# Kernel optimization log

Measured on AMD Instinct MI355X. Metric: run time of the kernel, lower is better.

Reference implementation:

```python
import jax, jax.numpy as jnp
import numpy as np
from jax import lax

T, D = 8192, 128          # sequence length, feature dim
N_INIT = 100              # burn-in length
RENORM = 0.1
A, B, C = 0.5, 0.9, 0.1   # weighted_dot scaling args: uv = A*gram + B*k_prev + C
EPS = 1e-6                # keep arcsin arg strictly inside (-1, 1)


def kernel_fn(uv, uu, vv):
    # erf-network arcsin kernel
    denom = jnp.sqrt((1.0 + 2.0 * uu) * (1.0 + 2.0 * vv))
    arg = jnp.clip(2.0 * uv / denom, -1.0 + EPS, 1.0 - EPS)
    return (2.0 / jnp.pi) * jnp.arcsin(arg)


def dot_fn(g, k):
    return A * g + B * k + C


def setup_inputs() -> dict:
    key = jax.random.key(0)
    data = jax.random.normal(key, (T, D), dtype=jnp.float32) / np.float32(np.sqrt(D))
    return {"data": data}


def reference(data):
    X = data[:-1]                      # [N, D], N = T - 1
    N = X.shape[0]
    gram = jnp.dot(X, X.T)             # [N, N]
    diag = jnp.diag(gram)              # [N]

    # --- diagonal recursion: scalar carry over time ---
    def diag_step(k_prev, g):
        uv = dot_fn(g, k_prev)
        k = kernel_fn(uv, uv, uv)
        return k, k

    k_diag_final, k_diag = lax.scan(diag_step, jnp.float32(0.0), diag)
    k_diag_shift = jnp.pad(k_diag[:-1], (1, 0))   # shift by one step
    uu = dot_fn(diag, k_diag_shift)               # [N]

    # --- full kernel recursion: carry is a length-N row, shifted each step ---
    def row_step(k_prev, inputs):
        g_row, vv = inputs
        k_prev = jnp.pad(k_prev[:-1], (1, 0))
        uv = dot_fn(g_row, k_prev)
        k = kernel_fn(uv, uu, vv)
        return k, k

    k_final, k_train = lax.scan(row_step, jnp.zeros((N,), jnp.float32), (gram, uu))

    k_train = k_train[N_INIT - 1:, N_INIT - 1:] + RENORM * gram[N_INIT - 1:, N_INIT - 1:]
    return (k_train, uu, k_final, k_diag_final)
```

## Files before the change

kernel.cpp:

```cpp
#include <hip/hip_runtime.h>
#include <hip/hip_fp16.h>

#define N_ROWS 8191
#define NO 8092
#define GSTRIDE 8192
#define SEG 512
#define WARM 96

#define OUT_UU  65480464ul
#define OUT_KF  65488655ul
#define OUT_KDF 65496846ul

#define WS_XB   134217728ul
#define WS_DIAG 136314880ul
#define WS_Q    136347648ul

typedef short bf16x8 __attribute__((ext_vector_type(8)));
typedef float f32x4  __attribute__((ext_vector_type(4)));

__device__ __forceinline__ float asin_core(float a) {
    float ax  = fabsf(a);
    bool  big = ax > 0.5f;
    float z   = big ? 0.5f * (1.0f - ax) : ax * ax;
    float x   = big ? sqrtf(z) : ax;
    float p = fmaf(z, 4.2163199048e-2f, 2.4181311049e-2f);
    p = fmaf(p, z, 4.5470025998e-2f);
    p = fmaf(p, z, 7.4953002686e-2f);
    p = fmaf(p, z, 1.6666752422e-1f);
    p = fmaf(p * z, x, x);
    float r = big ? fmaf(-2.0f, p, 1.57079632679489662f) : p;
    return copysignf(r, a);
}

__device__ __forceinline__ float kstep(float g, float kp, float m) {
    float uv  = fmaf(0.5f, g, fmaf(0.9f, kp, 0.1f));
    float arg = uv * m;
    arg = fminf(fmaxf(arg, -0.999999f), 0.999999f);
    return 0.63661977236758134f * asin_core(arg);
}

__device__ __forceinline__ unsigned short f2bf(float f) {
    unsigned int u = __float_as_uint(f);
    u = (u + 0x7FFFu + ((u >> 16) & 1u)) >> 16;
    return (unsigned short)u;
}

__global__ void k_convert(const float* __restrict__ X, unsigned short* __restrict__ Xb) {
    int idx = blockIdx.x * 256 + threadIdx.x;
    float v = (idx < N_ROWS * 128) ? X[idx] : 0.0f;
    Xb[idx] = f2bf(v);
}

__global__ void k_diag(const float* __restrict__ X, float* __restrict__ diag) {
    int gwave = (blockIdx.x * 256 + threadIdx.x) >> 6;
    int lane  = threadIdx.x & 63;
    if (gwave >= N_ROWS) return;
    const float2* row = (const float2*)(X + (size_t)gwave * 128);
    float2 v = row[lane];
    float s = v.x * v.x + v.y * v.y;
    #pragma unroll
    for (int off = 32; off > 0; off >>= 1) s += __shfl_xor(s, off, 64);
    if (lane == 0) diag[gwave] = s;
}

__global__ void k_scan_diag(const float* __restrict__ diag, float* __restrict__ q,
                            float* __restrict__ d_out) {
    int tid = threadIdx.x;
    int t0  = tid * 32;
    int tw  = max(0, t0 - 32);
    int te  = min(t0 + 32, N_ROWS);
    float kp = 0.0f;
    for (int t = tw; t < te; ++t) {
        float dg = diag[t];
        float uv = fmaf(0.5f, dg, fmaf(0.9f, kp, 0.1f));
        float s  = fabsf(fmaf(2.0f, uv, 1.0f));
        float arg = (uv + uv) / s;
        arg = fminf(fmaxf(arg, -0.999999f), 0.999999f);
        float k = 0.63661977236758134f * asin_core(arg);
        if (t >= t0) {
            d_out[OUT_UU + t] = uv;
            q[t] = 1.0f / sqrtf(s);
            if (t == N_ROWS - 1) d_out[OUT_KDF] = k;
        }
        kp = k;
    }
}

#define GP 136
__global__ __launch_bounds__(256) void k_gemm(const unsigned short* __restrict__ Xb,
                                              __half* __restrict__ gram) {
    int bi = blockIdx.y, bj = blockIdx.x;
    if (bj < bi) return;
    __shared__ short As[128 * GP];
    __shared__ short Bs[128 * GP];
    int tid = threadIdx.x;
    const uint4* ga = (const uint4*)(Xb + (size_t)bi * 128 * 128);
    const uint4* gb = (const uint4*)(Xb + (size_t)bj * 128 * 128);
    #pragma unroll
    for (int p = 0; p < 8; ++p) {
        int chunk = tid + p * 256;
        int row = chunk >> 4, c8 = chunk & 15;
        uint4 va = ga[row * 16 + c8];
        *(uint4*)&As[row * GP + c8 * 8] = va;
        uint4 vb = gb[row * 16 + c8];
        *(uint4*)&Bs[row * GP + c8 * 8] = vb;
    }
    __syncthreads();

    int lane = tid & 63, wave = tid >> 6;
    int wm = wave & 1, wn = wave >> 1;
    int lr = lane & 15, lk = lane >> 4;
    f32x4 acc[4][4];
    #pragma unroll
    for (int mi = 0; mi < 4; ++mi)
        #pragma unroll
        for (int ni = 0; ni < 4; ++ni) acc[mi][ni] = (f32x4){0.f, 0.f, 0.f, 0.f};

    #pragma unroll
    for (int kc = 0; kc < 4; ++kc) {
        bf16x8 a[4], b[4];
        #pragma unroll
        for (int mi = 0; mi < 4; ++mi)
            a[mi] = *(bf16x8*)&As[(wm * 64 + mi * 16 + lr) * GP + kc * 32 + lk * 8];
        #pragma unroll
        for (int ni = 0; ni < 4; ++ni)
            b[ni] = *(bf16x8*)&Bs[(wn * 64 + ni * 16 + lr) * GP + kc * 32 + lk * 8];
        #pragma unroll
        for (int mi = 0; mi < 4; ++mi)
            #pragma unroll
            for (int ni = 0; ni < 4; ++ni)
                acc[mi][ni] = __builtin_amdgcn_mfma_f32_16x16x32_bf16(a[mi], b[ni], acc[mi][ni], 0, 0, 0);
    }

    int row0 = (lane >> 4) * 4, col = lane & 15;
    #pragma unroll
    for (int mi = 0; mi < 4; ++mi) {
        #pragma unroll
        for (int ni = 0; ni < 4; ++ni) {
            size_t gi = (size_t)bi * 128 + wm * 64 + mi * 16 + row0;
            size_t gj = (size_t)bj * 128 + wn * 64 + ni * 16 + col;
            f32x4 v = acc[mi][ni];
            #pragma unroll
            for (int r = 0; r < 4; ++r)
                gram[(gi + r) * GSTRIDE + gj] = __float2half(v[r]);
        }
    }
}

__global__ __launch_bounds__(256) void k_scan_main(const __half* __restrict__ gram,
                                                   const float* __restrict__ q,
                                                   float* __restrict__ d_out) {
    int c = blockIdx.x * 256 + threadIdx.x;
    if (c > NO - 1) return;
    int tlim = N_ROWS - c;
    int t0 = 99 + blockIdx.y * SEG;
    if (t0 >= tlim) return;
    int tend = min(t0 + SEG, tlim);
    int tw = t0 - WARM;

    float kp = 0.0f;
    size_t gidx = (size_t)tw * GSTRIDE + tw + c;
    #pragma unroll 4
    for (int t = tw; t < t0; ++t, gidx += (GSTRIDE + 1)) {
        float g = __half2float(gram[gidx]);
        float m = 2.0f * q[t] * q[t + c];
        kp = kstep(g, kp, m);
    }
    size_t oidx = (size_t)(t0 - 99) * NO + (t0 + c - 99);
    #pragma unroll 4
    for (int t = t0; t < tend; ++t, gidx += (GSTRIDE + 1), oidx += (NO + 1)) {
        float g = __half2float(gram[gidx]);
        float m = 2.0f * q[t] * q[t + c];
        kp = kstep(g, kp, m);
        d_out[oidx] = fmaf(0.1f, g, kp);
    }
    if (tend == tlim) d_out[OUT_KF + (tlim - 1)] = kp;
}

__global__ void k_short_diag(const __half* __restrict__ gram, const float* __restrict__ q,
                             float* __restrict__ d_out) {
    int l = threadIdx.x;
    if (l > 98) return;
    int c = NO + l;
    int tl = N_ROWS - c;
    float kp = 0.0f;
    size_t gidx = (size_t)c;
    for (int t = 0; t < tl; ++t, gidx += (GSTRIDE + 1)) {
        float g = __half2float(gram[gidx]);
        float m = 2.0f * q[t] * q[t + c];
        kp = kstep(g, kp, m);
    }
    d_out[OUT_KF + (tl - 1)] = kp;
}

__global__ __launch_bounds__(256) void k_mirror(float* __restrict__ out) {
    int tc = blockIdx.x, tr = blockIdx.y;
    if (tr < tc) return;
    __shared__ float tile[32][33];
    int tx = threadIdx.x, ty = threadIdx.y;
    int sr0 = tc * 32, sc0 = tr * 32;
    #pragma unroll
    for (int k2 = 0; k2 < 32; k2 += 8) {
        int r = sr0 + ty + k2, cc = sc0 + tx;
        if (r < NO && cc < NO)
            tile[ty + k2][tx] = out[(size_t)r * NO + cc];
    }
    __syncthreads();
    int dr0 = tr * 32, dc0 = tc * 32;
    #pragma unroll
    for (int k2 = 0; k2 < 32; k2 += 8) {
        int r = dr0 + ty + k2, cc = dc0 + tx;
        if (r < NO && cc < NO && r > cc)
            out[(size_t)r * NO + cc] = tile[tx][ty + k2];
    }
}

extern "C" void kernel_launch(void* const* d_in, const int* in_sizes, int n_in,
                              void* d_out, int out_size, void* d_ws, size_t ws_size,
                              hipStream_t stream) {
    const float* X = (const float*)d_in[0];
    float* out = (float*)d_out;
    char* ws = (char*)d_ws;
    __half* gram = (__half*)ws;
    unsigned short* Xb = (unsigned short*)(ws + WS_XB);
    float* diag = (float*)(ws + WS_DIAG);
    float* q = (float*)(ws + WS_Q);

    k_convert<<<dim3(4096), dim3(256), 0, stream>>>(X, Xb);
    k_diag<<<dim3(2048), dim3(256), 0, stream>>>(X, diag);
    k_scan_diag<<<dim3(1), dim3(256), 0, stream>>>(diag, q, out);
    k_gemm<<<dim3(64, 64), dim3(256), 0, stream>>>(Xb, gram);
    k_scan_main<<<dim3(32, 16), dim3(256), 0, stream>>>(gram, q, out);
    k_short_diag<<<dim3(1), dim3(128), 0, stream>>>(gram, q, out);
    k_mirror<<<dim3(253, 253), dim3(32, 8), 0, stream>>>(out);
}
```

Measured before the change: 531.0 us.

## Fuse mirror write into scan via shared-memory transpose; merge convert and diag kernels

The scan kernel now stages its outputs in shared memory per 32-step chunk and writes the transposed lower-triangle entries directly. This removes the separate full-matrix mirror pass that re-read and rewrote the output. The bf16 conversion and diagonal norm kernels are merged into one launch, the factor of 2 is folded into q, and the warm-up length is halved. The costs are extra syncthreads and shared-memory traffic inside the scan, and a shorter warm-up that may lose accuracy.

```diff
diff --git a/kernel.cpp b/kernel.cpp
--- a/kernel.cpp
+++ b/kernel.cpp
@@ -5,7 +5,10 @@
 #define NO 8092
 #define GSTRIDE 8192
 #define SEG 512
-#define WARM 96
+#define WARM 48
+#define CHUNK 32
+#define LPAD 33
+#define LROWS (CHUNK + 255)
 
 #define OUT_UU  65480464ul
 #define OUT_KF  65488655ul
@@ -45,22 +48,23 @@
     return (unsigned short)u;
 }
 
-__global__ void k_convert(const float* __restrict__ X, unsigned short* __restrict__ Xb) {
-    int idx = blockIdx.x * 256 + threadIdx.x;
-    float v = (idx < N_ROWS * 128) ? X[idx] : 0.0f;
-    Xb[idx] = f2bf(v);
-}
-
-__global__ void k_diag(const float* __restrict__ X, float* __restrict__ diag) {
-    int gwave = (blockIdx.x * 256 + threadIdx.x) >> 6;
-    int lane  = threadIdx.x & 63;
-    if (gwave >= N_ROWS) return;
-    const float2* row = (const float2*)(X + (size_t)gwave * 128);
+__global__ void k_prep(const float* __restrict__ X, unsigned short* __restrict__ Xb,
+                       float* __restrict__ diag) {
+    int gw   = (blockIdx.x * 256 + threadIdx.x) >> 6;
+    int lane = threadIdx.x & 63;
+    unsigned int* Xb32 = (unsigned int*)Xb;
+    if (gw >= N_ROWS) {
+        Xb32[(size_t)gw * 64 + lane] = 0u;
+        return;
+    }
+    const float2* row = (const float2*)(X + (size_t)gw * 128);
     float2 v = row[lane];
-    float s = v.x * v.x + v.y * v.y;
+    unsigned int packed = (unsigned int)f2bf(v.x) | ((unsigned int)f2bf(v.y) << 16);
+    Xb32[(size_t)gw * 64 + lane] = packed;
+    float s = fmaf(v.x, v.x, v.y * v.y);
     #pragma unroll
     for (int off = 32; off > 0; off >>= 1) s += __shfl_xor(s, off, 64);
-    if (lane == 0) diag[gwave] = s;
+    if (lane == 0) diag[gw] = s;
 }
 
 __global__ void k_scan_diag(const float* __restrict__ diag, float* __restrict__ q,
@@ -79,11 +83,12 @@
         float k = 0.63661977236758134f * asin_core(arg);
         if (t >= t0) {
             d_out[OUT_UU + t] = uv;
-            q[t] = 1.0f / sqrtf(s);
+            q[t] = 1.41421356237309515f / sqrtf(s);
             if (t == N_ROWS - 1) d_out[OUT_KDF] = k;
         }
         kp = k;
     }
+    q[N_ROWS + tid] = 0.0f;
 }
 
 #define GP 136
@@ -150,31 +155,60 @@
 __global__ __launch_bounds__(256) void k_scan_main(const __half* __restrict__ gram,
                                                    const float* __restrict__ q,
                                                    float* __restrict__ d_out) {
-    int c = blockIdx.x * 256 + threadIdx.x;
-    if (c > NO - 1) return;
-    int tlim = N_ROWS - c;
-    int t0 = 99 + blockIdx.y * SEG;
-    if (t0 >= tlim) return;
-    int tend = min(t0 + SEG, tlim);
+    __shared__ float lt[LROWS * LPAD];
+    int tid = threadIdx.x;
+    int c0  = blockIdx.x * 256;
+    int t0  = 99 + blockIdx.y * SEG;
+    int tlim0 = N_ROWS - c0;
+    if (t0 >= tlim0) return;
+    int tmax = min(t0 + SEG, tlim0);
+    int c = c0 + tid;
+    int lane = tid & 63, wave = tid >> 6;
+    int sh = lane >> 5, l31 = lane & 31;
+
+    float kp = 0.0f;
     int tw = t0 - WARM;
-
-    float kp = 0.0f;
-    size_t gidx = (size_t)tw * GSTRIDE + tw + c;
+    size_t gidx = (size_t)tw * (GSTRIDE + 1) + (size_t)c;
     #pragma unroll 4
     for (int t = tw; t < t0; ++t, gidx += (GSTRIDE + 1)) {
         float g = __half2float(gram[gidx]);
-        float m = 2.0f * q[t] * q[t + c];
+        float m = q[t] * q[t + c];
         kp = kstep(g, kp, m);
     }
-    size_t oidx = (size_t)(t0 - 99) * NO + (t0 + c - 99);
-    #pragma unroll 4
-    for (int t = t0; t < tend; ++t, gidx += (GSTRIDE + 1), oidx += (NO + 1)) {
-        float g = __half2float(gram[gidx]);
-        float m = 2.0f * q[t] * q[t + c];
-        kp = kstep(g, kp, m);
-        d_out[oidx] = fmaf(0.1f, g, kp);
-    }
-    if (tend == tlim) d_out[OUT_KF + (tlim - 1)] = kp;
+
+    size_t oidx = (size_t)(t0 - 99) * NO + (size_t)(t0 + c - 99);
+    for (int tg = t0; tg < tmax; tg += CHUNK) {
+        int tch = min(CHUNK, tmax - tg);
+        #pragma unroll 4
+        for (int ti = 0; ti < tch; ++ti) {
+            int t = tg + ti;
+            float g = __half2float(gram[gidx]);
+            float m = q[t] * q[t + c];
+            kp = kstep(g, kp, m);
+            float v = fmaf(0.1f, g, kp);
+            lt[(ti + tid) * LPAD + ti] = v;
+            if (t + c < N_ROWS) {
+                d_out[oidx] = v;
+                if (t + c == N_ROWS - 1) d_out[OUT_KF + t] = kp;
+            }
+            gidx += (GSTRIDE + 1);
+            oidx += (NO + 1);
+        }
+        __syncthreads();
+        int smax  = tch + 255;
+        int rbase = tg + c0 - 99;
+        int cb    = tg - 99;
+        for (int sb = (wave << 1) + sh; sb < smax; sb += 8) {
+            int ti0 = max(0, sb - 255);
+            int tie = min(tch - 1, sb);
+            int t_i = ti0 + l31;
+            int row_g = rbase + sb;
+            if (t_i <= tie && row_g < NO && (sb - t_i + c0) > 0) {
+                d_out[(size_t)row_g * NO + (size_t)(cb + t_i)] = lt[sb * LPAD + t_i];
+            }
+        }
+        __syncthreads();
+    }
 }
 
 __global__ void k_short_diag(const __half* __restrict__ gram, const float* __restrict__ q,
@@ -187,32 +221,10 @@
     size_t gidx = (size_t)c;
     for (int t = 0; t < tl; ++t, gidx += (GSTRIDE + 1)) {
         float g = __half2float(gram[gidx]);
-        float m = 2.0f * q[t] * q[t + c];
+        float m = q[t] * q[t + c];
         kp = kstep(g, kp, m);
     }
     d_out[OUT_KF + (tl - 1)] = kp;
-}
-
-__global__ __launch_bounds__(256) void k_mirror(float* __restrict__ out) {
-    int tc = blockIdx.x, tr = blockIdx.y;
-    if (tr < tc) return;
-    __shared__ float tile[32][33];
-    int tx = threadIdx.x, ty = threadIdx.y;
-    int sr0 = tc * 32, sc0 = tr * 32;
-    #pragma unroll
-    for (int k2 = 0; k2 < 32; k2 += 8) {
-        int r = sr0 + ty + k2, cc = sc0 + tx;
-        if (r < NO && cc < NO)
-            tile[ty + k2][tx] = out[(size_t)r * NO + cc];
-    }
-    __syncthreads();
-    int dr0 = tr * 32, dc0 = tc * 32;
-    #pragma unroll
-    for (int k2 = 0; k2 < 32; k2 += 8) {
-        int r = dr0 + ty + k2, cc = dc0 + tx;
-        if (r < NO && cc < NO && r > cc)
-            out[(size_t)r * NO + cc] = tile[tx][ty + k2];
-    }
 }
 
 extern "C" void kernel_launch(void* const* d_in, const int* in_sizes, int n_in,
@@ -226,11 +238,9 @@
     float* diag = (float*)(ws + WS_DIAG);
     float* q = (float*)(ws + WS_Q);
 
-    k_convert<<<dim3(4096), dim3(256), 0, stream>>>(X, Xb);
-    k_diag<<<dim3(2048), dim3(256), 0, stream>>>(X, diag);
+    k_prep<<<dim3(2048), dim3(256), 0, stream>>>(X, Xb, diag);
     k_scan_diag<<<dim3(1), dim3(256), 0, stream>>>(diag, q, out);
     k_gemm<<<dim3(64, 64), dim3(256), 0, stream>>>(Xb, gram);
     k_scan_main<<<dim3(32, 16), dim3(256), 0, stream>>>(gram, q, out);
     k_short_diag<<<dim3(1), dim3(128), 0, stream>>>(gram, q, out);
-    k_mirror<<<dim3(253, 253), dim3(32, 8), 0, stream>>>(out);
-}
+}
```

New measurement: 721.8 us. 1.36x slower.
